# Performance work log

Hardware: AMD Instinct MI355X
Metric: run time of the kernel (lower is better)

Reference implementation:

```python
import jax, jax.numpy as jnp
import numpy as np

N_HEADS = 8
WINDOW = 64
NEG = -1e9


def _layer_norm(x, g, b, eps=1e-5):
    mu = jnp.mean(x, axis=-1, keepdims=True)
    var = jnp.mean((x - mu) ** 2, axis=-1, keepdims=True)
    return g * (x - mu) / jnp.sqrt(var + eps) + b


def _sinusoidal_pe(S, D):
    pos = jnp.arange(S, dtype=jnp.float32)[:, None]
    div = jnp.exp(jnp.arange(0, D, 2, dtype=jnp.float32) * (-jnp.log(jnp.float32(10000.0)) / D))
    pe = jnp.zeros((S, D), jnp.float32)
    pe = pe.at[:, 0::2].set(jnp.sin(pos * div))
    pe = pe.at[:, 1::2].set(jnp.cos(pos * div))
    return pe


def setup_inputs():
    key = jax.random.key(0)
    ks = jax.random.split(key, 8)
    L, S, D, DFF = 4, 2048, 1024, 2048
    p = lambda k, shape: jax.random.normal(k, shape, jnp.float32) * 0.02
    return {
        "T": 1800,
        "enc_inputs": jax.random.normal(ks[0], (1, S, D), jnp.float32),
        "global_idx": jax.random.randint(ks[1], (32,), 0, 27000),
        "Wq": p(ks[2], (L, D, D)),
        "Wk": p(ks[3], (L, D, D)),
        "Wv": p(ks[4], (L, D, D)),
        "Wo": p(ks[5], (L, D, D)),
        "ln1_g": jnp.ones((L, D), jnp.float32),
        "ln1_b": jnp.zeros((L, D), jnp.float32),
        "W1": p(ks[6], (L, D, DFF)),
        "W2": p(ks[7], (L, DFF, D)),
        "ln2_g": jnp.ones((L, D), jnp.float32),
        "ln2_b": jnp.zeros((L, D), jnp.float32),
    }


def reference(T, enc_inputs, global_idx, Wq, Wk, Wv, Wo, ln1_g, ln1_b, W1, W2, ln2_g, ln2_b):
    B, S, D = enc_inputs.shape
    L = Wq.shape[0]
    H, DK = N_HEADS, D // N_HEADS

    # enc_outputs = enc_inputs + PE(enc_inputs) = 2*enc_inputs + pe (faithful to source)
    pe = _sinusoidal_pe(S, D)
    x = enc_inputs + (enc_inputs + pe[None])

    # mask vector: 1 = local token, -1 = global token, 0 = pad
    idx = jnp.arange(S)
    mvec = jnp.where(idx < T, 1.0, 0.0)
    g = global_idx // 15
    valid = (g >= 0) & (g < S)
    is_global = jnp.any((idx[None, :] == g[:, None]) & valid[:, None], axis=0)
    mvec = jnp.where(is_global, jnp.float32(-1.0), mvec)

    half = WINDOW // 2
    local = jnp.abs(idx[:, None] - idx[None, :]) <= half
    nonpad = mvec != 0.0
    glob = mvec == -1.0
    allowed = nonpad[:, None] & nonpad[None, :] & (local | glob[:, None] | glob[None, :])
    scale = 1.0 / jnp.sqrt(jnp.float32(DK))

    for l in range(L):
        # local-global multi-head self-attention
        q = (x @ Wq[l]).reshape(B, S, H, DK).transpose(0, 2, 1, 3)
        k = (x @ Wk[l]).reshape(B, S, H, DK).transpose(0, 2, 1, 3)
        v = (x @ Wv[l]).reshape(B, S, H, DK).transpose(0, 2, 1, 3)
        scores = jnp.einsum("bhqd,bhkd->bhqk", q, k) * scale
        scores = jnp.where(allowed[None, None], scores, jnp.float32(NEG))
        attn = jax.nn.softmax(scores, axis=-1)
        ctx = jnp.einsum("bhqk,bhkd->bhqd", attn, v).transpose(0, 2, 1, 3).reshape(B, S, D)
        x = _layer_norm(ctx @ Wo[l] + x, ln1_g[l], ln1_b[l])
        # position-wise FFN with residual + LayerNorm
        h = jax.nn.relu(x @ W1[l]) @ W2[l]
        x = _layer_norm(h + x, ln2_g[l], ln2_b[l])

    return x[0]  # squeeze(0): (S, D)
```

## Files before the change

kernel.cpp:

```cpp
#include <hip/hip_runtime.h>
#include <cstdint>
#include <cstddef>

#define S_LEN  2048
#define D_MODEL 1024
#define D_FF   2048
#define NLAYER 4

typedef float  f32x4  __attribute__((ext_vector_type(4)));
typedef __bf16 bf16x8 __attribute__((ext_vector_type(8)));

#define ATT_SCALE 0.08838834764831845f

__device__ __forceinline__ void async_copy16(const void* g, void* s) {
    __builtin_amdgcn_global_load_lds((const __attribute__((address_space(1))) void*)g,
                                     (__attribute__((address_space(3))) void*)s, 16, 0, 0);
}

template<int NW>
__device__ __forceinline__ float blockRedSum(float v, float* red) {
    #pragma unroll
    for (int off = 32; off > 0; off >>= 1) v += __shfl_down(v, off);
    const int t = threadIdx.x;
    if ((t & 63) == 0) red[t >> 6] = v;
    __syncthreads();
    float r = red[0];
    #pragma unroll
    for (int i = 1; i < NW; i++) r += red[i];
    __syncthreads();
    return r;
}

__global__ __launch_bounds__(256)
void init_mask_kernel(const float* __restrict__ enc, float* __restrict__ x,
                      __bf16* __restrict__ xb, const int* __restrict__ gidx,
                      int* __restrict__ isg, int* __restrict__ gcols, int* __restrict__ ngc) {
    const int t = threadIdx.x;
    if (blockIdx.x < S_LEN) {
        const int s = blockIdx.x;
        #pragma unroll
        for (int i = 0; i < 4; i++) {
            const int d = t + i * 256;
            const float freq = expf(-(float)(d & ~1) * (9.210340371976184f / 1024.0f));
            const float ang = (float)s * freq;
            const float pe = (d & 1) ? cosf(ang) : sinf(ang);
            const float v = 2.0f * enc[(size_t)s * D_MODEL + d] + pe;
            x[(size_t)s * D_MODEL + d] = v;
            xb[(size_t)s * D_MODEL + d] = (__bf16)v;
        }
    } else {
        __shared__ int gsh[32];
        __shared__ int cnt;
        if (t < 32) {
            const int g = gidx[t] / 15;
            gsh[t] = (g >= 0 && g < S_LEN) ? g : -1;
        }
        if (t == 0) cnt = 0;
        __syncthreads();
        #pragma unroll
        for (int i = 0; i < 8; i++) {
            const int s = t + i * 256;
            int f = 0;
            #pragma unroll
            for (int j = 0; j < 32; j++) f |= (gsh[j] == s) ? 1 : 0;
            isg[s] = f;
            if (f) { const int p = atomicAdd(&cnt, 1); gcols[p] = s; }
        }
        __syncthreads();
        if (t == 0) *ngc = cnt;
    }
}

__global__ __launch_bounds__(256)
void transpose_all_kernel(const float* __restrict__ Wq, const float* __restrict__ Wk,
                          const float* __restrict__ Wv, const float* __restrict__ Wo,
                          const float* __restrict__ W1, const float* __restrict__ W2,
                          __bf16* __restrict__ out, float* __restrict__ vmean) {
    int bid = blockIdx.x;
    if (bid < 4) vmean[bid * 256 + threadIdx.x] = 0.0f;
    const float* in; __bf16* o; int K, N, r;
    if (bid < 4096) {
        const int m = bid >> 10; r = bid & 1023; K = 1024; N = 1024;
        in = (m == 0) ? Wq : (m == 1) ? Wk : (m == 2) ? Wv : Wo;
        o  = out + (size_t)m * 1024 * 1024;
    } else {
        bid -= 4096;
        const int m = bid >> 11; r = bid & 2047;
        if (m == 0) { in = W1; K = 1024; N = 2048; o = out + (size_t)4 * 1024 * 1024; }
        else        { in = W2; K = 2048; N = 1024; o = out + (size_t)6 * 1024 * 1024; }
    }
    const int ntx = N >> 5;
    const int n0 = (r % ntx) * 32, k0 = (r / ntx) * 32;
    __shared__ float tile[32][33];
    const int tx = threadIdx.x & 31, ty = threadIdx.x >> 5;
    #pragma unroll
    for (int i = ty; i < 32; i += 8)
        tile[i][tx] = in[(size_t)(k0 + i) * N + n0 + tx];
    __syncthreads();
    #pragma unroll
    for (int i = ty; i < 32; i += 8)
        o[(size_t)(n0 + i) * K + k0 + tx] = (__bf16)tile[tx][i];
}

template<int BM, int BN, int EPI, bool VACC>
__global__ __launch_bounds__(256)
void gemm_bt(const __bf16* __restrict__ A, const __bf16* __restrict__ Bt,
             void* __restrict__ Cv, float* __restrict__ vmean, int M, int N, int K) {
    constexpr int WM = BM / 2, WN = BN / 2;
    constexpr int MI = WM / 16, NI = WN / 16;
    __shared__ __bf16 As[BM * 64];
    __shared__ __bf16 Bs[BN * 64];
    const int t = threadIdx.x;
    const int w = t >> 6, l = t & 63;
    const int l15 = l & 15, q4 = l >> 4;
    const int wr = w >> 1, wc = w & 1;
    const int m0 = blockIdx.y * BM, n0 = blockIdx.x * BN;

    const int srow = t >> 3;
    const int kc8  = (t & 7) * 8;
    const __bf16* ag = A  + (size_t)(m0 + srow) * K + kc8;
    const __bf16* bg = Bt + (size_t)(n0 + srow) * K + kc8;
    __bf16* asw = As + w * 512;
    __bf16* bsw = Bs + w * 512;

    const int aoff = (wr * WM + l15) * 64 + q4 * 8;
    const int boff = (wc * WN + l15) * 64 + q4 * 8;

    f32x4 acc[MI][NI];
    #pragma unroll
    for (int i = 0; i < MI; i++)
        #pragma unroll
        for (int j = 0; j < NI; j++) acc[i][j] = (f32x4){0.f, 0.f, 0.f, 0.f};

    for (int k0 = 0; k0 < K; k0 += 64) {
        async_copy16(ag + k0, asw);
        async_copy16(ag + (size_t)32 * K + k0, asw + 2048);
        if constexpr (BM == 128) {
            async_copy16(ag + (size_t)64 * K + k0, asw + 4096);
            async_copy16(ag + (size_t)96 * K + k0, asw + 6144);
        }
        async_copy16(bg + k0, bsw);
        async_copy16(bg + (size_t)32 * K + k0, bsw + 2048);
        if constexpr (BN == 128) {
            async_copy16(bg + (size_t)64 * K + k0, bsw + 4096);
            async_copy16(bg + (size_t)96 * K + k0, bsw + 6144);
        }
        __syncthreads();
        #pragma unroll
        for (int s = 0; s < 64; s += 32) {
            bf16x8 af[MI], bfr[NI];
            #pragma unroll
            for (int i = 0; i < MI; i++) af[i]  = *(const bf16x8*)(As + aoff + i * 1024 + s);
            #pragma unroll
            for (int j = 0; j < NI; j++) bfr[j] = *(const bf16x8*)(Bs + boff + j * 1024 + s);
            #pragma unroll
            for (int i = 0; i < MI; i++)
                #pragma unroll
                for (int j = 0; j < NI; j++)
                    acc[i][j] = __builtin_amdgcn_mfma_f32_16x16x32_bf16(af[i], bfr[j], acc[i][j], 0, 0, 0);
        }
        __syncthreads();
    }

    const int r0 = m0 + wr * WM + q4 * 4;
    const int c0 = n0 + wc * WN + l15;
    if constexpr (EPI == 0) {
        float* C = (float*)Cv;
        #pragma unroll
        for (int i = 0; i < MI; i++)
            #pragma unroll
            for (int j = 0; j < NI; j++)
                #pragma unroll
                for (int r = 0; r < 4; r++)
                    C[(size_t)(r0 + i * 16 + r) * N + c0 + j * 16] = acc[i][j][r];
    } else if constexpr (EPI == 1) {
        __bf16* C = (__bf16*)Cv;
        #pragma unroll
// ... 12 lines not shown
                #pragma unroll
                for (int r = 0; r < 4; r++)
                    C[(size_t)(r0 + i * 16 + r) * N + c0 + j * 16] = (__bf16)acc[i][j][r];
    }
    if constexpr (VACC) {
        #pragma unroll
        for (int j = 0; j < NI; j++) {
            const int col = c0 + j * 16;
            if (col >= 2048) {
                float s = 0.f;
                #pragma unroll
                for (int i = 0; i < MI; i++)
                    #pragma unroll
                    for (int r = 0; r < 4; r++) s += acc[i][j][r];
                s += __shfl_xor(s, 16);
                s += __shfl_xor(s, 32);
                if (q4 == 0) atomicAdd(&vmean[col - 2048], s);
            }
        }
    }
}

__global__ __launch_bounds__(256)
void attn_local(const __bf16* __restrict__ qkvb, const int* __restrict__ Tp,
                const int* __restrict__ isg, const int* __restrict__ gcols,
                const int* __restrict__ ngcp, const float* __restrict__ vmean,
                __bf16* __restrict__ ctx) {
    const int qt0 = blockIdx.x * 32, h = blockIdx.y, hd = h * 128;
    const int t = threadIdx.x;
    __shared__ __bf16 Qs[32 * 136];
    __shared__ __bf16 Ks[128 * 136];
    __shared__ __bf16 Vs[128 * 136];
    __shared__ __bf16 Ps[32 * 136];
    __shared__ float  Ss[32 * 129];
    __shared__ int cix[128], cgf[128], rtype[32];
    __shared__ int ncs;
    const int T = *Tp, ng = *ngcp;
    const int wl = max(qt0 - 32, 0), wh = min(qt0 + 63, S_LEN - 1);
    if (t == 0) ncs = 0;
    if (t < 32) { const int qr = qt0 + t; rtype[t] = isg[qr] ? 1 : (qr < T ? 0 : 2); }
    __syncthreads();
    if (t <= wh - wl) {
        const int c = wl + t, gf = isg[c];
        if (c < T || gf) { const int p = atomicAdd(&ncs, 1); cix[p] = c; cgf[p] = gf; }
    }
    if (t < ng) {
        const int c = gcols[t];
        if (c < wl || c > wh) { const int p = atomicAdd(&ncs, 1); cix[p] = c; cgf[p] = 1; }
    }
    {
        const int r = t >> 3, d0 = (t & 7) * 16;
        const bf16x8* src = (const bf16x8*)(qkvb + (size_t)(qt0 + r) * 3072 + hd + d0);
        *(bf16x8*)&Qs[r * 136 + d0]     = src[0];
        *(bf16x8*)&Qs[r * 136 + d0 + 8] = src[1];
    }
    __syncthreads();
    const int nc = ncs;
    if (nc + t < 128) { cix[nc + t] = -1; cgf[nc + t] = 0; }
    {
        const int j = t >> 1, d0 = (t & 1) * 64;
        const int ci = (j < nc) ? cix[j] : -1;
        if (ci >= 0) {
            const bf16x8* kp = (const bf16x8*)(qkvb + (size_t)ci * 3072 + 1024 + hd + d0);
            const bf16x8* vp = (const bf16x8*)(qkvb + (size_t)ci * 3072 + 2048 + hd + d0);
            #pragma unroll
            for (int i = 0; i < 8; i++) {
                *(bf16x8*)&Ks[j * 136 + d0 + i * 8] = kp[i];
                *(bf16x8*)&Vs[j * 136 + d0 + i * 8] = vp[i];
            }
        } else {
            #pragma unroll
            for (int i = 0; i < 8; i++) {
                *(bf16x8*)&Ks[j * 136 + d0 + i * 8] = (bf16x8)(__bf16)0.f;
                *(bf16x8*)&Vs[j * 136 + d0 + i * 8] = (bf16x8)(__bf16)0.f;
            }
        }
    }
    __syncthreads();

    const int l = t & 63, w = t >> 6;
    const int l15 = l & 15, q4 = l >> 4;
    const int nb = w * 32;
    {
        f32x4 sacc[2][2];
        #pragma unroll
        for (int i = 0; i < 2; i++)
            #pragma unroll
            for (int j = 0; j < 2; j++) sacc[i][j] = (f32x4){0.f, 0.f, 0.f, 0.f};
        #pragma unroll
        for (int kk = 0; kk < 4; kk++) {
            const int k0 = kk * 32;
            bf16x8 af[2], bk[2];
            af[0] = *(const bf16x8*)&Qs[l15 * 136 + k0 + q4 * 8];
            af[1] = *(const bf16x8*)&Qs[(16 + l15) * 136 + k0 + q4 * 8];
            bk[0] = *(const bf16x8*)&Ks[(nb + l15) * 136 + k0 + q4 * 8];
            bk[1] = *(const bf16x8*)&Ks[(nb + 16 + l15) * 136 + k0 + q4 * 8];
            #pragma unroll
            for (int m2 = 0; m2 < 2; m2++)
                #pragma unroll
                for (int n2 = 0; n2 < 2; n2++)
                    sacc[m2][n2] = __builtin_amdgcn_mfma_f32_16x16x32_bf16(af[m2], bk[n2], sacc[m2][n2], 0, 0, 0);
        }
        #pragma unroll
        for (int m2 = 0; m2 < 2; m2++)
            #pragma unroll
            for (int n2 = 0; n2 < 2; n2++)
                #pragma unroll
                for (int r = 0; r < 4; r++) {
                    const int row = m2 * 16 + q4 * 4 + r;
                    const int col = nb + n2 * 16 + l15;
                    const int c = cix[col];
                    const int dd = qt0 + row - c;
                    const bool ok = (c >= 0) && (((unsigned)(dd + 32) <= 64u) || cgf[col]);
                    Ss[row * 129 + col] = ok ? sacc[m2][n2][r] * ATT_SCALE : -1e30f;
                }
    }
    __syncthreads();
    {
        const int r = t >> 3, i = t & 7;
        float mx = -1e30f;
        for (int c = i; c < 128; c += 8) mx = fmaxf(mx, Ss[r * 129 + c]);
        #pragma unroll
        for (int off = 4; off > 0; off >>= 1) mx = fmaxf(mx, __shfl_down(mx, off, 8));
        mx = __shfl(mx, 0, 8);
        float sm = 0.f;
        for (int c = i; c < 128; c += 8) {
            const float s = Ss[r * 129 + c];
            const float p = (s > -1e29f) ? __expf(s - mx) : 0.f;
            Ss[r * 129 + c] = p;
            sm += p;
        }
        #pragma unroll
        for (int off = 4; off > 0; off >>= 1) sm += __shfl_down(sm, off, 8);
        sm = __shfl(sm, 0, 8);
        const float rl = 1.0f / fmaxf(sm, 1e-30f);
        for (int c = i; c < 128; c += 8) Ps[r * 136 + c] = (__bf16)(Ss[r * 129 + c] * rl);
    }
    __syncthreads();
    {
        f32x4 oacc[2][2];
        #pragma unroll
        for (int i = 0; i < 2; i++)
            #pragma unroll
            for (int j = 0; j < 2; j++) oacc[i][j] = (f32x4){0.f, 0.f, 0.f, 0.f};
        #pragma unroll
        for (int kk = 0; kk < 4; kk++) {
            const int k0 = kk * 32;
            bf16x8 ap[2], bv[2];
            ap[0] = *(const bf16x8*)&Ps[l15 * 136 + k0 + q4 * 8];
            ap[1] = *(const bf16x8*)&Ps[(16 + l15) * 136 + k0 + q4 * 8];
            #pragma unroll
            for (int n2 = 0; n2 < 2; n2++) {
                const int dimn = nb + n2 * 16 + l15;
                #pragma unroll
                for (int jj = 0; jj < 8; jj++)
                    bv[n2][jj] = Vs[(k0 + q4 * 8 + jj) * 136 + dimn];
            }
            #pragma unroll
            for (int m2 = 0; m2 < 2; m2++)
                #pragma unroll
                for (int n2 = 0; n2 < 2; n2++)
                    oacc[m2][n2] = __builtin_amdgcn_mfma_f32_16x16x32_bf16(ap[m2], bv[n2], oacc[m2][n2], 0, 0, 0);
        }
        #pragma unroll
        for (int m2 = 0; m2 < 2; m2++)
            #pragma unroll
            for (int n2 = 0; n2 < 2; n2++)
                #pragma unroll
                for (int r = 0; r < 4; r++) {
                    const int row = m2 * 16 + q4 * 4 + r;
                    const int dim = nb + n2 * 16 + l15;
                    const int rt = rtype[row];
                    const size_t o = (size_t)(qt0 + row) * D_MODEL + hd + dim;
                    if (rt == 0)      ctx[o] = (__bf16)oacc[m2][n2][r];
                    else if (rt == 2) ctx[o] = (__bf16)(vmean[hd + dim] * (1.0f / 2048.0f));
                }
    }
}

__global__ __launch_bounds__(256)
void attn_gpart(const __bf16* __restrict__ qkvb, const int* __restrict__ Tp,
                const int* __restrict__ isg, const int* __restrict__ gcols,
                const int* __restrict__ ngcp, float* __restrict__ Og,
                float* __restrict__ mg, float* __restrict__ lg) {
    const int cb = blockIdx.x, h = blockIdx.y, hd = h * 128, c0 = cb * 128;
    const int t = threadIdx.x;
    const int ng = *ngcp, T = *Tp;
    if (ng == 0) return;
    __shared__ __bf16 Qs[32 * 136];
    __shared__ __bf16 Ks[128 * 136];
    __shared__ __bf16 Vs[128 * 136];
    __shared__ __bf16 Ps[32 * 136];
    __shared__ float  Ss[32 * 129];
    __shared__ int vf[128];
    {
        const int r = t >> 3, d0 = (t & 7) * 16;
        if (r < ng) {
            const bf16x8* src = (const bf16x8*)(qkvb + (size_t)gcols[r] * 3072 + hd + d0);
            *(bf16x8*)&Qs[r * 136 + d0]     = src[0];
            *(bf16x8*)&Qs[r * 136 + d0 + 8] = src[1];
        } else {
            *(bf16x8*)&Qs[r * 136 + d0]     = (bf16x8)(__bf16)0.f;
            *(bf16x8*)&Qs[r * 136 + d0 + 8] = (bf16x8)(__bf16)0.f;
        }
    }
    if (t < 128) { const int c = c0 + t; vf[t] = (c < T || isg[c]) ? 1 : 0; }
    {
        const int j = t >> 1, d0 = (t & 1) * 64;
        const int ci = c0 + j;
        const bf16x8* kp = (const bf16x8*)(qkvb + (size_t)ci * 3072 + 1024 + hd + d0);
        const bf16x8* vp = (const bf16x8*)(qkvb + (size_t)ci * 3072 + 2048 + hd + d0);
        #pragma unroll
        for (int i = 0; i < 8; i++) {
            *(bf16x8*)&Ks[j * 136 + d0 + i * 8] = kp[i];
            *(bf16x8*)&Vs[j * 136 + d0 + i * 8] = vp[i];
        }
    }
    __syncthreads();

    const int l = t & 63, w = t >> 6;
    const int l15 = l & 15, q4 = l >> 4;
    const int nb = w * 32;
    {
        f32x4 sacc[2][2];
        #pragma unroll
        for (int i = 0; i < 2; i++)
            #pragma unroll
            for (int j = 0; j < 2; j++) sacc[i][j] = (f32x4){0.f, 0.f, 0.f, 0.f};
        #pragma unroll
        for (int kk = 0; kk < 4; kk++) {
            const int k0 = kk * 32;
            bf16x8 af[2], bk[2];
            af[0] = *(const bf16x8*)&Qs[l15 * 136 + k0 + q4 * 8];
            af[1] = *(const bf16x8*)&Qs[(16 + l15) * 136 + k0 + q4 * 8];
            bk[0] = *(const bf16x8*)&Ks[(nb + l15) * 136 + k0 + q4 * 8];
            bk[1] = *(const bf16x8*)&Ks[(nb + 16 + l15) * 136 + k0 + q4 * 8];
            #pragma unroll
            for (int m2 = 0; m2 < 2; m2++)
                #pragma unroll
                for (int n2 = 0; n2 < 2; n2++)
                    sacc[m2][n2] = __builtin_amdgcn_mfma_f32_16x16x32_bf16(af[m2], bk[n2], sacc[m2][n2], 0, 0, 0);
        }
        #pragma unroll
        for (int m2 = 0; m2 < 2; m2++)
            #pragma unroll
            for (int n2 = 0; n2 < 2; n2++)
                #pragma unroll
                for (int r = 0; r < 4; r++) {
                    const int row = m2 * 16 + q4 * 4 + r;
                    const int col = nb + n2 * 16 + l15;
                    Ss[row * 129 + col] = vf[col] ? sacc[m2][n2][r] * ATT_SCALE : -1e30f;
                }
    }
    __syncthreads();
    {
        const int r = t >> 3, i = t & 7;
        float mx = -1e30f;
        for (int c = i; c < 128; c += 8) mx = fmaxf(mx, Ss[r * 129 + c]);
        #pragma unroll
        for (int off = 4; off > 0; off >>= 1) mx = fmaxf(mx, __shfl_down(mx, off, 8));
        mx = __shfl(mx, 0, 8);
        float sm = 0.f;
        for (int c = i; c < 128; c += 8) {
            const float s = Ss[r * 129 + c];
            const float p = (s > -1e29f) ? __expf(s - mx) : 0.f;
            Ps[r * 136 + c] = (__bf16)p;
            sm += p;
        }
        #pragma unroll
        for (int off = 4; off > 0; off >>= 1) sm += __shfl_down(sm, off, 8);
        if (i == 0) { mg[(h * 16 + cb) * 32 + r] = mx; lg[(h * 16 + cb) * 32 + r] = sm; }
    }
    __syncthreads();
    {
        f32x4 oacc[2][2];
        #pragma unroll
        for (int i = 0; i < 2; i++)
            #pragma unroll
            for (int j = 0; j < 2; j++) oacc[i][j] = (f32x4){0.f, 0.f, 0.f, 0.f};
        #pragma unroll
        for (int kk = 0; kk < 4; kk++) {
            const int k0 = kk * 32;
            bf16x8 ap[2], bv[2];
            ap[0] = *(const bf16x8*)&Ps[l15 * 136 + k0 + q4 * 8];
            ap[1] = *(const bf16x8*)&Ps[(16 + l15) * 136 + k0 + q4 * 8];
            #pragma unroll
            for (int n2 = 0; n2 < 2; n2++) {
                const int dimn = nb + n2 * 16 + l15;
                #pragma unroll
                for (int jj = 0; jj < 8; jj++)
                    bv[n2][jj] = Vs[(k0 + q4 * 8 + jj) * 136 + dimn];
            }
            #pragma unroll
            for (int m2 = 0; m2 < 2; m2++)
                #pragma unroll
                for (int n2 = 0; n2 < 2; n2++)
                    oacc[m2][n2] = __builtin_amdgcn_mfma_f32_16x16x32_bf16(ap[m2], bv[n2], oacc[m2][n2], 0, 0, 0);
        }
        #pragma unroll
        for (int m2 = 0; m2 < 2; m2++)
            #pragma unroll
            for (int n2 = 0; n2 < 2; n2++)
                #pragma unroll
                for (int r = 0; r < 4; r++) {
                    const int row = m2 * 16 + q4 * 4 + r;
                    const int dim = nb + n2 * 16 + l15;
                    Og[((size_t)(h * 16 + cb) * 32 + row) * 128 + dim] = oacc[m2][n2][r];
                }
    }
}

__global__ __launch_bounds__(256)
void attn_gcomb(const int* __restrict__ gcols, const int* __restrict__ ngcp,
                const float* __restrict__ Og, const float* __restrict__ mg,
                const float* __restrict__ lg, __bf16* __restrict__ ctx) {
    const int h = blockIdx.x, hd = h * 128, t = threadIdx.x;
    const int ng = *ngcp;
    const int r = t >> 3, i = t & 7;
    if (r >= ng) return;
    float M = -1e30f;
    #pragma unroll
    for (int cb = 0; cb < 16; cb++) M = fmaxf(M, mg[(h * 16 + cb) * 32 + r]);
    float e[16], L = 0.f;
    #pragma unroll
    for (int cb = 0; cb < 16; cb++) {
        e[cb] = __expf(mg[(h * 16 + cb) * 32 + r] - M);
        L += e[cb] * lg[(h * 16 + cb) * 32 + r];
    }
    const float rL = 1.0f / fmaxf(L, 1e-30f);
    const int grow = gcols[r];
    for (int d = i; d < 128; d += 8) {
        float o = 0.f;
        #pragma unroll
        for (int cb = 0; cb < 16; cb++)
            o += e[cb] * Og[((size_t)(h * 16 + cb) * 32 + r) * 128 + d];
        ctx[(size_t)grow * D_MODEL + hd + d] = (__bf16)(o * rL);
    }
}

__global__ __launch_bounds__(256)
void ln_kernel(const float* __restrict__ y, const float* __restrict__ r,
               const float* __restrict__ g, const float* __restrict__ b,
               float* __restrict__ xo, __bf16* __restrict__ xb) {
    const int row = blockIdx.x, t = threadIdx.x;
    const float* yr = y + (size_t)row * D_MODEL;
    const float* rr = r + (size_t)row * D_MODEL;
    __shared__ float red[4];
    float v[4]; float s = 0.f;
    #pragma unroll
    for (int i = 0; i < 4; i++) { const int d = t + i * 256; v[i] = yr[d] + rr[d]; s += v[i]; }
    s = blockRedSum<4>(s, red);
    const float mu = s * (1.0f / 1024.0f);
    float vs = 0.f;
    #pragma unroll
    for (int i = 0; i < 4; i++) { const float dd = v[i] - mu; vs += dd * dd; }
    vs = blockRedSum<4>(vs, red);
    const float rstd = rsqrtf(vs * (1.0f / 1024.0f) + 1e-5f);
    #pragma unroll
    for (int i = 0; i < 4; i++) {
        const int d = t + i * 256;
        const float o = g[d] * (v[i] - mu) * rstd + b[d];
        xo[(size_t)row * D_MODEL + d] = o;
        xb[(size_t)row * D_MODEL + d] = (__bf16)o;
    }
}

extern "C" void kernel_launch(void* const* d_in, const int* in_sizes, int n_in,
// ... 6 lines not shown
    const float* Wk   = (const float*)d_in[4];
    const float* Wv   = (const float*)d_in[5];
    const float* Wo   = (const float*)d_in[6];
    const float* ln1g = (const float*)d_in[7];
    const float* ln1b = (const float*)d_in[8];
    const float* W1   = (const float*)d_in[9];
    const float* W2   = (const float*)d_in[10];
    const float* ln2g = (const float*)d_in[11];
    const float* ln2b = (const float*)d_in[12];

    char* p = (char*)d_ws;
    size_t off = 0;
    auto alloc = [&](size_t bytes) -> void* {
        void* q = p + off;
        off += (bytes + 255) & ~(size_t)255;
        return q;
    };
    float*  x     = (float*) alloc((size_t)S_LEN * D_MODEL * 4);
    __bf16* xb    = (__bf16*)alloc((size_t)S_LEN * D_MODEL * 2);
    __bf16* qkvb  = (__bf16*)alloc((size_t)S_LEN * 3072 * 2);
    __bf16* ctx   = (__bf16*)alloc((size_t)S_LEN * D_MODEL * 2);
    float*  g1    = (float*) alloc((size_t)S_LEN * D_MODEL * 4);
    __bf16* h1    = (__bf16*)alloc((size_t)S_LEN * D_FF * 2);
    __bf16* wT    = (__bf16*)alloc((size_t)8 * 1024 * 1024 * 2);
    float*  vmean = (float*) alloc(1024 * 4);
    int*    isg   = (int*)   alloc(S_LEN * 4);
    int*    gcols = (int*)   alloc(S_LEN * 4);
    int*    ngc   = (int*)   alloc(256);
    float*  Og    = (float*) alloc((size_t)8 * 16 * 32 * 128 * 4);
    float*  mgb   = (float*) alloc(8 * 16 * 32 * 4);
    float*  lgb   = (float*) alloc(8 * 16 * 32 * 4);

    init_mask_kernel<<<S_LEN + 1, 256, 0, stream>>>(enc, x, xb, gidx, isg, gcols, ngc);

    for (int l = 0; l < NLAYER; l++) {
        const size_t lw = (size_t)l * 1024 * 1024;
        const size_t lf = (size_t)l * 1024 * 2048;
        transpose_all_kernel<<<8192, 256, 0, stream>>>(Wq + lw, Wk + lw, Wv + lw, Wo + lw,
                                                       W1 + lf, W2 + lf, wT, vmean);
        gemm_bt<64, 128, 2, true><<<dim3(24, 32), 256, 0, stream>>>(xb, wT, (void*)qkvb, vmean, S_LEN, 3072, 1024);

        attn_local<<<dim3(64, 8), 256, 0, stream>>>(qkvb, Tp, isg, gcols, ngc, vmean, ctx);
        attn_gpart<<<dim3(16, 8), 256, 0, stream>>>(qkvb, Tp, isg, gcols, ngc, Og, mgb, lgb);
        attn_gcomb<<<8, 256, 0, stream>>>(gcols, ngc, Og, mgb, lgb, ctx);

        gemm_bt<64, 64, 0, false><<<dim3(16, 32), 256, 0, stream>>>(ctx, wT + (size_t)3 * 1024 * 1024, (void*)g1, nullptr, S_LEN, 1024, 1024);
        ln_kernel<<<S_LEN, 256, 0, stream>>>(g1, x, ln1g + l * 1024, ln1b + l * 1024, x, xb);

        gemm_bt<64, 64, 1, false><<<dim3(32, 32), 256, 0, stream>>>(xb, wT + (size_t)4 * 1024 * 1024, (void*)h1, nullptr, S_LEN, 2048, 1024);
        gemm_bt<64, 64, 0, false><<<dim3(16, 32), 256, 0, stream>>>(h1, wT + (size_t)6 * 1024 * 1024, (void*)g1, nullptr, S_LEN, 1024, 2048);
        float* xout = (l == NLAYER - 1) ? (float*)d_out : x;
        ln_kernel<<<S_LEN, 256, 0, stream>>>(g1, x, ln2g + l * 1024, ln2b + l * 1024, xout, xb);
    }
}
```

Baseline: 768.6 us.

## Batch weight transposes, fuse attention kernels, and deepen GEMM K-tile

Transposes all four layers' weights in one upfront launch into a larger arena instead of once per layer. The local and global-partial attention kernels are merged into a single launch, and vmean zeroing moves into the init and LayerNorm kernels. The GEMM K-tile grows from 64 to 128 through a new template parameter. These cut launch count and per-iteration sync overhead, but the larger LDS tiles may lower occupancy and the weight arena now takes four times the memory.

```diff
diff --git a/kernel.cpp b/kernel.cpp
--- a/kernel.cpp
+++ b/kernel.cpp
@@ -34,7 +34,8 @@
 __global__ __launch_bounds__(256)
 void init_mask_kernel(const float* __restrict__ enc, float* __restrict__ x,
                       __bf16* __restrict__ xb, const int* __restrict__ gidx,
-                      int* __restrict__ isg, int* __restrict__ gcols, int* __restrict__ ngc) {
+                      int* __restrict__ isg, int* __restrict__ gcols, int* __restrict__ ngc,
+                      float* __restrict__ vmean) {
     const int t = threadIdx.x;
     if (blockIdx.x < S_LEN) {
         const int s = blockIdx.x;
@@ -49,6 +50,8 @@
             xb[(size_t)s * D_MODEL + d] = (__bf16)v;
         }
     } else {
+        #pragma unroll
+        for (int i = 0; i < 4; i++) vmean[t + i * 256] = 0.0f;
         __shared__ int gsh[32];
         __shared__ int cnt;
         if (t < 32) {
@@ -75,19 +78,22 @@
 void transpose_all_kernel(const float* __restrict__ Wq, const float* __restrict__ Wk,
                           const float* __restrict__ Wv, const float* __restrict__ Wo,
                           const float* __restrict__ W1, const float* __restrict__ W2,
-                          __bf16* __restrict__ out, float* __restrict__ vmean) {
-    int bid = blockIdx.x;
-    if (bid < 4) vmean[bid * 256 + threadIdx.x] = 0.0f;
+                          __bf16* __restrict__ out) {
+    const int layer = blockIdx.x >> 13;
+    int bid = blockIdx.x & 8191;
+    const size_t lw = (size_t)layer * 1024 * 1024;
+    const size_t lf = (size_t)layer * 1024 * 2048;
+    __bf16* arena = out + (size_t)layer * 8 * 1024 * 1024;
     const float* in; __bf16* o; int K, N, r;
     if (bid < 4096) {
         const int m = bid >> 10; r = bid & 1023; K = 1024; N = 1024;
-        in = (m == 0) ? Wq : (m == 1) ? Wk : (m == 2) ? Wv : Wo;
-        o  = out + (size_t)m * 1024 * 1024;
+        in = ((m == 0) ? Wq : (m == 1) ? Wk : (m == 2) ? Wv : Wo) + lw;
+        o  = arena + (size_t)m * 1024 * 1024;
     } else {
         bid -= 4096;
         const int m = bid >> 11; r = bid & 2047;
-        if (m == 0) { in = W1; K = 1024; N = 2048; o = out + (size_t)4 * 1024 * 1024; }
-        else        { in = W2; K = 2048; N = 1024; o = out + (size_t)6 * 1024 * 1024; }
+        if (m == 0) { in = W1 + lf; K = 1024; N = 2048; o = arena + (size_t)4 * 1024 * 1024; }
+        else        { in = W2 + lf; K = 2048; N = 1024; o = arena + (size_t)6 * 1024 * 1024; }
     }
     const int ntx = N >> 5;
     const int n0 = (r % ntx) * 32, k0 = (r / ntx) * 32;
@@ -102,29 +108,32 @@
         o[(size_t)(n0 + i) * K + k0 + tx] = (__bf16)tile[tx][i];
 }
 
-template<int BM, int BN, int EPI, bool VACC>
+template<int BM, int BN, int BK, int EPI, bool VACC>
 __global__ __launch_bounds__(256)
 void gemm_bt(const __bf16* __restrict__ A, const __bf16* __restrict__ Bt,
              void* __restrict__ Cv, float* __restrict__ vmean, int M, int N, int K) {
     constexpr int WM = BM / 2, WN = BN / 2;
     constexpr int MI = WM / 16, NI = WN / 16;
-    __shared__ __bf16 As[BM * 64];
-    __shared__ __bf16 Bs[BN * 64];
+    constexpr int TPR = BK / 8;
+    constexpr int RPR = 2048 / BK;
+    constexpr int RA = BM / RPR, RB = BN / RPR;
+    __shared__ __bf16 As[BM * BK];
+    __shared__ __bf16 Bs[BN * BK];
     const int t = threadIdx.x;
     const int w = t >> 6, l = t & 63;
     const int l15 = l & 15, q4 = l >> 4;
     const int wr = w >> 1, wc = w & 1;
     const int m0 = blockIdx.y * BM, n0 = blockIdx.x * BN;
 
-    const int srow = t >> 3;
-    const int kc8  = (t & 7) * 8;
+    const int srow = t / TPR;
+    const int kc8  = (t % TPR) * 8;
     const __bf16* ag = A  + (size_t)(m0 + srow) * K + kc8;
     const __bf16* bg = Bt + (size_t)(n0 + srow) * K + kc8;
     __bf16* asw = As + w * 512;
     __bf16* bsw = Bs + w * 512;
 
-    const int aoff = (wr * WM + l15) * 64 + q4 * 8;
-    const int boff = (wc * WN + l15) * 64 + q4 * 8;
+    const int aoff = (wr * WM + l15) * BK + q4 * 8;
+    const int boff = (wc * WN + l15) * BK + q4 * 8;
 
     f32x4 acc[MI][NI];
     #pragma unroll
@@ -132,27 +141,21 @@
         #pragma unroll
         for (int j = 0; j < NI; j++) acc[i][j] = (f32x4){0.f, 0.f, 0.f, 0.f};
 
-    for (int k0 = 0; k0 < K; k0 += 64) {
-        async_copy16(ag + k0, asw);
-        async_copy16(ag + (size_t)32 * K + k0, asw + 2048);
-        if constexpr (BM == 128) {
-            async_copy16(ag + (size_t)64 * K + k0, asw + 4096);
-            async_copy16(ag + (size_t)96 * K + k0, asw + 6144);
-        }
-        async_copy16(bg + k0, bsw);
-        async_copy16(bg + (size_t)32 * K + k0, bsw + 2048);
-        if constexpr (BN == 128) {
-            async_copy16(bg + (size_t)64 * K + k0, bsw + 4096);
-            async_copy16(bg + (size_t)96 * K + k0, bsw + 6144);
-        }
-        __syncthreads();
-        #pragma unroll
-        for (int s = 0; s < 64; s += 32) {
+    for (int k0 = 0; k0 < K; k0 += BK) {
+        #pragma unroll
+        for (int rr = 0; rr < RA; rr++)
+            async_copy16(ag + (size_t)rr * RPR * K + k0, asw + rr * 2048);
+        #pragma unroll
+        for (int rr = 0; rr < RB; rr++)
+            async_copy16(bg + (size_t)rr * RPR * K + k0, bsw + rr * 2048);
+        __syncthreads();
+        #pragma unroll
+        for (int s = 0; s < BK; s += 32) {
             bf16x8 af[MI], bfr[NI];
             #pragma unroll
-            for (int i = 0; i < MI; i++) af[i]  = *(const bf16x8*)(As + aoff + i * 1024 + s);
-            #pragma unroll
-            for (int j = 0; j < NI; j++) bfr[j] = *(const bf16x8*)(Bs + boff + j * 1024 + s);
+            for (int i = 0; i < MI; i++) af[i]  = *(const bf16x8*)(As + aoff + i * 16 * BK + s);
+            #pragma unroll
+            for (int j = 0; j < NI; j++) bfr[j] = *(const bf16x8*)(Bs + boff + j * 16 * BK + s);
             #pragma unroll
             for (int i = 0; i < MI; i++)
                 #pragma unroll
@@ -211,12 +214,14 @@
 }
 
 __global__ __launch_bounds__(256)
-void attn_local(const __bf16* __restrict__ qkvb, const int* __restrict__ Tp,
-                const int* __restrict__ isg, const int* __restrict__ gcols,
-                const int* __restrict__ ngcp, const float* __restrict__ vmean,
-                __bf16* __restrict__ ctx) {
-    const int qt0 = blockIdx.x * 32, h = blockIdx.y, hd = h * 128;
+void attn_kernel(const __bf16* __restrict__ qkvb, const int* __restrict__ Tp,
+                 const int* __restrict__ isg, const int* __restrict__ gcols,
+                 const int* __restrict__ ngcp, const float* __restrict__ vmean,
+                 __bf16* __restrict__ ctx, float* __restrict__ Og,
+                 float* __restrict__ mg, float* __restrict__ lg) {
+    const int h = blockIdx.y, hd = h * 128;
     const int t = threadIdx.x;
+    const int T = *Tp, ng = *ngcp;
     __shared__ __bf16 Qs[32 * 136];
     __shared__ __bf16 Ks[128 * 136];
     __shared__ __bf16 Vs[128 * 136];
@@ -224,32 +229,166 @@
     __shared__ float  Ss[32 * 129];
     __shared__ int cix[128], cgf[128], rtype[32];
     __shared__ int ncs;
-    const int T = *Tp, ng = *ngcp;
-    const int wl = max(qt0 - 32, 0), wh = min(qt0 + 63, S_LEN - 1);
-    if (t == 0) ncs = 0;
-    if (t < 32) { const int qr = qt0 + t; rtype[t] = isg[qr] ? 1 : (qr < T ? 0 : 2); }
-    __syncthreads();
-    if (t <= wh - wl) {
-        const int c = wl + t, gf = isg[c];
-        if (c < T || gf) { const int p = atomicAdd(&ncs, 1); cix[p] = c; cgf[p] = gf; }
-    }
-    if (t < ng) {
-        const int c = gcols[t];
-        if (c < wl || c > wh) { const int p = atomicAdd(&ncs, 1); cix[p] = c; cgf[p] = 1; }
-    }
-    {
-        const int r = t >> 3, d0 = (t & 7) * 16;
-        const bf16x8* src = (const bf16x8*)(qkvb + (size_t)(qt0 + r) * 3072 + hd + d0);
-        *(bf16x8*)&Qs[r * 136 + d0]     = src[0];
-        *(bf16x8*)&Qs[r * 136 + d0 + 8] = src[1];
-    }
-    __syncthreads();
-    const int nc = ncs;
-    if (nc + t < 128) { cix[nc + t] = -1; cgf[nc + t] = 0; }
-    {
-        const int j = t >> 1, d0 = (t & 1) * 64;
-        const int ci = (j < nc) ? cix[j] : -1;
-        if (ci >= 0) {
+    const int l = t & 63, w = t >> 6;
+    const int l15 = l & 15, q4 = l >> 4;
+    const int nb = w * 32;
+
+    if (blockIdx.x < 64) {
+        const int qt0 = blockIdx.x * 32;
+        const int wl = max(qt0 - 32, 0), wh = min(qt0 + 63, S_LEN - 1);
+        if (t == 0) ncs = 0;
+        if (t < 32) { const int qr = qt0 + t; rtype[t] = isg[qr] ? 1 : (qr < T ? 0 : 2); }
+        __syncthreads();
+        if (t <= wh - wl) {
+            const int c = wl + t, gf = isg[c];
+            if (c < T || gf) { const int p = atomicAdd(&ncs, 1); cix[p] = c; cgf[p] = gf; }
+        }
+        if (t < ng) {
+            const int c = gcols[t];
+            if (c < wl || c > wh) { const int p = atomicAdd(&ncs, 1); cix[p] = c; cgf[p] = 1; }
+        }
+        {
+            const int r = t >> 3, d0 = (t & 7) * 16;
+            const bf16x8* src = (const bf16x8*)(qkvb + (size_t)(qt0 + r) * 3072 + hd + d0);
+            *(bf16x8*)&Qs[r * 136 + d0]     = src[0];
+            *(bf16x8*)&Qs[r * 136 + d0 + 8] = src[1];
+        }
+        __syncthreads();
+        const int nc = ncs;
+        if (nc + t < 128) { cix[nc + t] = -1; cgf[nc + t] = 0; }
+        {
+            const int j = t >> 1, d0 = (t & 1) * 64;
+            const int ci = (j < nc) ? cix[j] : -1;
+            if (ci >= 0) {
+                const bf16x8* kp = (const bf16x8*)(qkvb + (size_t)ci * 3072 + 1024 + hd + d0);
+                const bf16x8* vp = (const bf16x8*)(qkvb + (size_t)ci * 3072 + 2048 + hd + d0);
+                #pragma unroll
+                for (int i = 0; i < 8; i++) {
+                    *(bf16x8*)&Ks[j * 136 + d0 + i * 8] = kp[i];
+                    *(bf16x8*)&Vs[j * 136 + d0 + i * 8] = vp[i];
+                }
+            } else {
+                #pragma unroll
+                for (int i = 0; i < 8; i++) {
+                    *(bf16x8*)&Ks[j * 136 + d0 + i * 8] = (bf16x8)(__bf16)0.f;
+                    *(bf16x8*)&Vs[j * 136 + d0 + i * 8] = (bf16x8)(__bf16)0.f;
+                }
+            }
+        }
+        __syncthreads();
+        {
+            f32x4 sacc[2][2];
+            #pragma unroll
+            for (int i = 0; i < 2; i++)
+                #pragma unroll
+                for (int j = 0; j < 2; j++) sacc[i][j] = (f32x4){0.f, 0.f, 0.f, 0.f};
+            #pragma unroll
+            for (int kk = 0; kk < 4; kk++) {
+                const int k0 = kk * 32;
+                bf16x8 af[2], bk[2];
+                af[0] = *(const bf16x8*)&Qs[l15 * 136 + k0 + q4 * 8];
+                af[1] = *(const bf16x8*)&Qs[(16 + l15) * 136 + k0 + q4 * 8];
+                bk[0] = *(const bf16x8*)&Ks[(nb + l15) * 136 + k0 + q4 * 8];
+                bk[1] = *(const bf16x8*)&Ks[(nb + 16 + l15) * 136 + k0 + q4 * 8];
+                #pragma unroll
+                for (int m2 = 0; m2 < 2; m2++)
+                    #pragma unroll
+                    for (int n2 = 0; n2 < 2; n2++)
+                        sacc[m2][n2] = __builtin_amdgcn_mfma_f32_16x16x32_bf16(af[m2], bk[n2], sacc[m2][n2], 0, 0, 0);
+            }
+            #pragma unroll
+            for (int m2 = 0; m2 < 2; m2++)
+                #pragma unroll
+                for (int n2 = 0; n2 < 2; n2++)
+                    #pragma unroll
+                    for (int r = 0; r < 4; r++) {
+                        const int row = m2 * 16 + q4 * 4 + r;
+                        const int col = nb + n2 * 16 + l15;
+                        const int c = cix[col];
+                        const int dd = qt0 + row - c;
+                        const bool ok = (c >= 0) && (((unsigned)(dd + 32) <= 64u) || cgf[col]);
+                        Ss[row * 129 + col] = ok ? sacc[m2][n2][r] * ATT_SCALE : -1e30f;
+                    }
+        }
+        __syncthreads();
+        {
+            const int r = t >> 3, i = t & 7;
+            float mx = -1e30f;
+            for (int c = i; c < 128; c += 8) mx = fmaxf(mx, Ss[r * 129 + c]);
+            #pragma unroll
+            for (int off = 4; off > 0; off >>= 1) mx = fmaxf(mx, __shfl_down(mx, off, 8));
+            mx = __shfl(mx, 0, 8);
+            float sm = 0.f;
+            for (int c = i; c < 128; c += 8) {
+                const float s = Ss[r * 129 + c];
+                const float p = (s > -1e29f) ? __expf(s - mx) : 0.f;
+                Ss[r * 129 + c] = p;
+                sm += p;
+            }
+            #pragma unroll
+            for (int off = 4; off > 0; off >>= 1) sm += __shfl_down(sm, off, 8);
+            sm = __shfl(sm, 0, 8);
+            const float rl = 1.0f / fmaxf(sm, 1e-30f);
+            for (int c = i; c < 128; c += 8) Ps[r * 136 + c] = (__bf16)(Ss[r * 129 + c] * rl);
+        }
+        __syncthreads();
+        {
+            f32x4 oacc[2][2];
+            #pragma unroll
+            for (int i = 0; i < 2; i++)
+                #pragma unroll
+                for (int j = 0; j < 2; j++) oacc[i][j] = (f32x4){0.f, 0.f, 0.f, 0.f};
+            #pragma unroll
+            for (int kk = 0; kk < 4; kk++) {
+                const int k0 = kk * 32;
+                bf16x8 ap[2], bv[2];
+                ap[0] = *(const bf16x8*)&Ps[l15 * 136 + k0 + q4 * 8];
+                ap[1] = *(const bf16x8*)&Ps[(16 + l15) * 136 + k0 + q4 * 8];
+                #pragma unroll
+                for (int n2 = 0; n2 < 2; n2++) {
+                    const int dimn = nb + n2 * 16 + l15;
+                    #pragma unroll
+                    for (int jj = 0; jj < 8; jj++)
+                        bv[n2][jj] = Vs[(k0 + q4 * 8 + jj) * 136 + dimn];
+                }
+                #pragma unroll
+                for (int m2 = 0; m2 < 2; m2++)
+                    #pragma unroll
+                    for (int n2 = 0; n2 < 2; n2++)
+                        oacc[m2][n2] = __builtin_amdgcn_mfma_f32_16x16x32_bf16(ap[m2], bv[n2], oacc[m2][n2], 0, 0, 0);
+            }
+            #pragma unroll
+            for (int m2 = 0; m2 < 2; m2++)
+                #pragma unroll
+                for (int n2 = 0; n2 < 2; n2++)
+                    #pragma unroll
+                    for (int r = 0; r < 4; r++) {
+                        const int row = m2 * 16 + q4 * 4 + r;
+                        const int dim = nb + n2 * 16 + l15;
+                        const int rt = rtype[row];
+                        const size_t o = (size_t)(qt0 + row) * D_MODEL + hd + dim;
+                        if (rt == 0)      ctx[o] = (__bf16)oacc[m2][n2][r];
+                        else if (rt == 2) ctx[o] = (__bf16)(vmean[hd + dim] * (1.0f / 2048.0f));
+                    }
+        }
+    } else {
+        if (ng == 0) return;
+        const int cb = blockIdx.x - 64, c0 = cb * 128;
+        {
+            const int r = t >> 3, d0 = (t & 7) * 16;
+            if (r < ng) {
+                const bf16x8* src = (const bf16x8*)(qkvb + (size_t)gcols[r] * 3072 + hd + d0);
+                *(bf16x8*)&Qs[r * 136 + d0]     = src[0];
+                *(bf16x8*)&Qs[r * 136 + d0 + 8] = src[1];
+            } else {
+                *(bf16x8*)&Qs[r * 136 + d0]     = (bf16x8)(__bf16)0.f;
+                *(bf16x8*)&Qs[r * 136 + d0 + 8] = (bf16x8)(__bf16)0.f;
+            }
+        }
+        if (t < 128) { const int c = c0 + t; cix[t] = (c < T || isg[c]) ? 1 : 0; }
+        {
+            const int j = t >> 1, d0 = (t & 1) * 64;
+            const int ci = c0 + j;
             const bf16x8* kp = (const bf16x8*)(qkvb + (size_t)ci * 3072 + 1024 + hd + d0);
             const bf16x8* vp = (const bf16x8*)(qkvb + (size_t)ci * 3072 + 2048 + hd + d0);
             #pragma unroll
@@ -257,245 +396,95 @@
                 *(bf16x8*)&Ks[j * 136 + d0 + i * 8] = kp[i];
                 *(bf16x8*)&Vs[j * 136 + d0 + i * 8] = vp[i];
             }
-        } else {
-            #pragma unroll
-            for (int i = 0; i < 8; i++) {
-                *(bf16x8*)&Ks[j * 136 + d0 + i * 8] = (bf16x8)(__bf16)0.f;
-                *(bf16x8*)&Vs[j * 136 + d0 + i * 8] = (bf16x8)(__bf16)0.f;
-            }
-        }
-    }
-    __syncthreads();
-
-    const int l = t & 63, w = t >> 6;
-    const int l15 = l & 15, q4 = l >> 4;
-    const int nb = w * 32;
-    {
-        f32x4 sacc[2][2];
-        #pragma unroll
-        for (int i = 0; i < 2; i++)
-            #pragma unroll
-            for (int j = 0; j < 2; j++) sacc[i][j] = (f32x4){0.f, 0.f, 0.f, 0.f};
-        #pragma unroll
-        for (int kk = 0; kk < 4; kk++) {
-            const int k0 = kk * 32;
-            bf16x8 af[2], bk[2];
-            af[0] = *(const bf16x8*)&Qs[l15 * 136 + k0 + q4 * 8];
-            af[1] = *(const bf16x8*)&Qs[(16 + l15) * 136 + k0 + q4 * 8];
-            bk[0] = *(const bf16x8*)&Ks[(nb + l15) * 136 + k0 + q4 * 8];
-            bk[1] = *(const bf16x8*)&Ks[(nb + 16 + l15) * 136 + k0 + q4 * 8];
+        }
+        __syncthreads();
+        {
+            f32x4 sacc[2][2];
+            #pragma unroll
+            for (int i = 0; i < 2; i++)
+                #pragma unroll
+                for (int j = 0; j < 2; j++) sacc[i][j] = (f32x4){0.f, 0.f, 0.f, 0.f};
+            #pragma unroll
+            for (int kk = 0; kk < 4; kk++) {
+                const int k0 = kk * 32;
+                bf16x8 af[2], bk[2];
+                af[0] = *(const bf16x8*)&Qs[l15 * 136 + k0 + q4 * 8];
+                af[1] = *(const bf16x8*)&Qs[(16 + l15) * 136 + k0 + q4 * 8];
+                bk[0] = *(const bf16x8*)&Ks[(nb + l15) * 136 + k0 + q4 * 8];
+                bk[1] = *(const bf16x8*)&Ks[(nb + 16 + l15) * 136 + k0 + q4 * 8];
+                #pragma unroll
+                for (int m2 = 0; m2 < 2; m2++)
+                    #pragma unroll
+                    for (int n2 = 0; n2 < 2; n2++)
+                        sacc[m2][n2] = __builtin_amdgcn_mfma_f32_16x16x32_bf16(af[m2], bk[n2], sacc[m2][n2], 0, 0, 0);
+            }
             #pragma unroll
             for (int m2 = 0; m2 < 2; m2++)
                 #pragma unroll
                 for (int n2 = 0; n2 < 2; n2++)
-                    sacc[m2][n2] = __builtin_amdgcn_mfma_f32_16x16x32_bf16(af[m2], bk[n2], sacc[m2][n2], 0, 0, 0);
-        }
-        #pragma unroll
-        for (int m2 = 0; m2 < 2; m2++)
-            #pragma unroll
-            for (int n2 = 0; n2 < 2; n2++)
-                #pragma unroll
-                for (int r = 0; r < 4; r++) {
-                    const int row = m2 * 16 + q4 * 4 + r;
-                    const int col = nb + n2 * 16 + l15;
-                    const int c = cix[col];
-                    const int dd = qt0 + row - c;
-                    const bool ok = (c >= 0) && (((unsigned)(dd + 32) <= 64u) || cgf[col]);
-                    Ss[row * 129 + col] = ok ? sacc[m2][n2][r] * ATT_SCALE : -1e30f;
+                    #pragma unroll
+                    for (int r = 0; r < 4; r++) {
+                        const int row = m2 * 16 + q4 * 4 + r;
+                        const int col = nb + n2 * 16 + l15;
+                        Ss[row * 129 + col] = cix[col] ? sacc[m2][n2][r] * ATT_SCALE : -1e30f;
+                    }
+        }
+        __syncthreads();
+        {
+            const int r = t >> 3, i = t & 7;
+            float mx = -1e30f;
+            for (int c = i; c < 128; c += 8) mx = fmaxf(mx, Ss[r * 129 + c]);
+            #pragma unroll
+            for (int off = 4; off > 0; off >>= 1) mx = fmaxf(mx, __shfl_down(mx, off, 8));
+            mx = __shfl(mx, 0, 8);
+            float sm = 0.f;
+            for (int c = i; c < 128; c += 8) {
+                const float s = Ss[r * 129 + c];
+                const float p = (s > -1e29f) ? __expf(s - mx) : 0.f;
+                Ps[r * 136 + c] = (__bf16)p;
+                sm += p;
+            }
+            #pragma unroll
+            for (int off = 4; off > 0; off >>= 1) sm += __shfl_down(sm, off, 8);
+            if (i == 0) { mg[(h * 16 + cb) * 32 + r] = mx; lg[(h * 16 + cb) * 32 + r] = sm; }
+        }
+        __syncthreads();
+        {
+            f32x4 oacc[2][2];
+            #pragma unroll
+            for (int i = 0; i < 2; i++)
+                #pragma unroll
+                for (int j = 0; j < 2; j++) oacc[i][j] = (f32x4){0.f, 0.f, 0.f, 0.f};
+            #pragma unroll
+            for (int kk = 0; kk < 4; kk++) {
+                const int k0 = kk * 32;
+                bf16x8 ap[2], bv[2];
+                ap[0] = *(const bf16x8*)&Ps[l15 * 136 + k0 + q4 * 8];
+                ap[1] = *(const bf16x8*)&Ps[(16 + l15) * 136 + k0 + q4 * 8];
+                #pragma unroll
+                for (int n2 = 0; n2 < 2; n2++) {
+                    const int dimn = nb + n2 * 16 + l15;
+                    #pragma unroll
+                    for (int jj = 0; jj < 8; jj++)
+                        bv[n2][jj] = Vs[(k0 + q4 * 8 + jj) * 136 + dimn];
                 }
-    }
-    __syncthreads();
-    {
-        const int r = t >> 3, i = t & 7;
-        float mx = -1e30f;
-        for (int c = i; c < 128; c += 8) mx = fmaxf(mx, Ss[r * 129 + c]);
-        #pragma unroll
-        for (int off = 4; off > 0; off >>= 1) mx = fmaxf(mx, __shfl_down(mx, off, 8));
-        mx = __shfl(mx, 0, 8);
-        float sm = 0.f;
-        for (int c = i; c < 128; c += 8) {
-            const float s = Ss[r * 129 + c];
-            const float p = (s > -1e29f) ? __expf(s - mx) : 0.f;
-            Ss[r * 129 + c] = p;
-            sm += p;
-        }
-        #pragma unroll
-        for (int off = 4; off > 0; off >>= 1) sm += __shfl_down(sm, off, 8);
-        sm = __shfl(sm, 0, 8);
-        const float rl = 1.0f / fmaxf(sm, 1e-30f);
-        for (int c = i; c < 128; c += 8) Ps[r * 136 + c] = (__bf16)(Ss[r * 129 + c] * rl);
-    }
-    __syncthreads();
-    {
-        f32x4 oacc[2][2];
-        #pragma unroll
-        for (int i = 0; i < 2; i++)
-            #pragma unroll
-            for (int j = 0; j < 2; j++) oacc[i][j] = (f32x4){0.f, 0.f, 0.f, 0.f};
-        #pragma unroll
-        for (int kk = 0; kk < 4; kk++) {
-            const int k0 = kk * 32;
-            bf16x8 ap[2], bv[2];
-            ap[0] = *(const bf16x8*)&Ps[l15 * 136 + k0 + q4 * 8];
-            ap[1] = *(const bf16x8*)&Ps[(16 + l15) * 136 + k0 + q4 * 8];
-            #pragma unroll
-            for (int n2 = 0; n2 < 2; n2++) {
-                const int dimn = nb + n2 * 16 + l15;
-                #pragma unroll
-                for (int jj = 0; jj < 8; jj++)
-                    bv[n2][jj] = Vs[(k0 + q4 * 8 + jj) * 136 + dimn];
+                #pragma unroll
+                for (int m2 = 0; m2 < 2; m2++)
+                    #pragma unroll
+                    for (int n2 = 0; n2 < 2; n2++)
+                        oacc[m2][n2] = __builtin_amdgcn_mfma_f32_16x16x32_bf16(ap[m2], bv[n2], oacc[m2][n2], 0, 0, 0);
             }
             #pragma unroll
             for (int m2 = 0; m2 < 2; m2++)
                 #pragma unroll
                 for (int n2 = 0; n2 < 2; n2++)
-                    oacc[m2][n2] = __builtin_amdgcn_mfma_f32_16x16x32_bf16(ap[m2], bv[n2], oacc[m2][n2], 0, 0, 0);
-        }
-        #pragma unroll
-        for (int m2 = 0; m2 < 2; m2++)
-            #pragma unroll
-            for (int n2 = 0; n2 < 2; n2++)
-                #pragma unroll
-                for (int r = 0; r < 4; r++) {
-                    const int row = m2 * 16 + q4 * 4 + r;
-                    const int dim = nb + n2 * 16 + l15;
-                    const int rt = rtype[row];
-                    const size_t o = (size_t)(qt0 + row) * D_MODEL + hd + dim;
-                    if (rt == 0)      ctx[o] = (__bf16)oacc[m2][n2][r];
-                    else if (rt == 2) ctx[o] = (__bf16)(vmean[hd + dim] * (1.0f / 2048.0f));
-                }
-    }
-}
-
-__global__ __launch_bounds__(256)
-void attn_gpart(const __bf16* __restrict__ qkvb, const int* __restrict__ Tp,
-                const int* __restrict__ isg, const int* __restrict__ gcols,
-                const int* __restrict__ ngcp, float* __restrict__ Og,
-                float* __restrict__ mg, float* __restrict__ lg) {
-    const int cb = blockIdx.x, h = blockIdx.y, hd = h * 128, c0 = cb * 128;
-    const int t = threadIdx.x;
-    const int ng = *ngcp, T = *Tp;
-    if (ng == 0) return;
-    __shared__ __bf16 Qs[32 * 136];
-    __shared__ __bf16 Ks[128 * 136];
-    __shared__ __bf16 Vs[128 * 136];
-    __shared__ __bf16 Ps[32 * 136];
-    __shared__ float  Ss[32 * 129];
-    __shared__ int vf[128];
-    {
-        const int r = t >> 3, d0 = (t & 7) * 16;
-        if (r < ng) {
-            const bf16x8* src = (const bf16x8*)(qkvb + (size_t)gcols[r] * 3072 + hd + d0);
-            *(bf16x8*)&Qs[r * 136 + d0]     = src[0];
-            *(bf16x8*)&Qs[r * 136 + d0 + 8] = src[1];
-        } else {
-            *(bf16x8*)&Qs[r * 136 + d0]     = (bf16x8)(__bf16)0.f;
-            *(bf16x8*)&Qs[r * 136 + d0 + 8] = (bf16x8)(__bf16)0.f;
-        }
-    }
-    if (t < 128) { const int c = c0 + t; vf[t] = (c < T || isg[c]) ? 1 : 0; }
-    {
-        const int j = t >> 1, d0 = (t & 1) * 64;
-        const int ci = c0 + j;
-        const bf16x8* kp = (const bf16x8*)(qkvb + (size_t)ci * 3072 + 1024 + hd + d0);
-        const bf16x8* vp = (const bf16x8*)(qkvb + (size_t)ci * 3072 + 2048 + hd + d0);
-        #pragma unroll
-        for (int i = 0; i < 8; i++) {
-            *(bf16x8*)&Ks[j * 136 + d0 + i * 8] = kp[i];
-            *(bf16x8*)&Vs[j * 136 + d0 + i * 8] = vp[i];
-        }
-    }
-    __syncthreads();
-
-    const int l = t & 63, w = t >> 6;
-    const int l15 = l & 15, q4 = l >> 4;
-    const int nb = w * 32;
-    {
-        f32x4 sacc[2][2];
-        #pragma unroll
-        for (int i = 0; i < 2; i++)
-            #pragma unroll
-            for (int j = 0; j < 2; j++) sacc[i][j] = (f32x4){0.f, 0.f, 0.f, 0.f};
-        #pragma unroll
-        for (int kk = 0; kk < 4; kk++) {
-            const int k0 = kk * 32;
-            bf16x8 af[2], bk[2];
-            af[0] = *(const bf16x8*)&Qs[l15 * 136 + k0 + q4 * 8];
-            af[1] = *(const bf16x8*)&Qs[(16 + l15) * 136 + k0 + q4 * 8];
-            bk[0] = *(const bf16x8*)&Ks[(nb + l15) * 136 + k0 + q4 * 8];
-            bk[1] = *(const bf16x8*)&Ks[(nb + 16 + l15) * 136 + k0 + q4 * 8];
-            #pragma unroll
-            for (int m2 = 0; m2 < 2; m2++)
-                #pragma unroll
-                for (int n2 = 0; n2 < 2; n2++)
-                    sacc[m2][n2] = __builtin_amdgcn_mfma_f32_16x16x32_bf16(af[m2], bk[n2], sacc[m2][n2], 0, 0, 0);
-        }
-        #pragma unroll
-        for (int m2 = 0; m2 < 2; m2++)
-            #pragma unroll
-            for (int n2 = 0; n2 < 2; n2++)
-                #pragma unroll
-                for (int r = 0; r < 4; r++) {
-                    const int row = m2 * 16 + q4 * 4 + r;
-                    const int col = nb + n2 * 16 + l15;
-                    Ss[row * 129 + col] = vf[col] ? sacc[m2][n2][r] * ATT_SCALE : -1e30f;
-                }
-    }
-    __syncthreads();
-    {
-        const int r = t >> 3, i = t & 7;
-        float mx = -1e30f;
-        for (int c = i; c < 128; c += 8) mx = fmaxf(mx, Ss[r * 129 + c]);
-        #pragma unroll
-        for (int off = 4; off > 0; off >>= 1) mx = fmaxf(mx, __shfl_down(mx, off, 8));
-        mx = __shfl(mx, 0, 8);
-        float sm = 0.f;
-        for (int c = i; c < 128; c += 8) {
-            const float s = Ss[r * 129 + c];
-            const float p = (s > -1e29f) ? __expf(s - mx) : 0.f;
-            Ps[r * 136 + c] = (__bf16)p;
-            sm += p;
-        }
-        #pragma unroll
-        for (int off = 4; off > 0; off >>= 1) sm += __shfl_down(sm, off, 8);
-        if (i == 0) { mg[(h * 16 + cb) * 32 + r] = mx; lg[(h * 16 + cb) * 32 + r] = sm; }
-    }
-    __syncthreads();
-    {
-        f32x4 oacc[2][2];
-        #pragma unroll
-        for (int i = 0; i < 2; i++)
-            #pragma unroll
-            for (int j = 0; j < 2; j++) oacc[i][j] = (f32x4){0.f, 0.f, 0.f, 0.f};
-        #pragma unroll
-        for (int kk = 0; kk < 4; kk++) {
-            const int k0 = kk * 32;
-            bf16x8 ap[2], bv[2];
-            ap[0] = *(const bf16x8*)&Ps[l15 * 136 + k0 + q4 * 8];
-            ap[1] = *(const bf16x8*)&Ps[(16 + l15) * 136 + k0 + q4 * 8];
-            #pragma unroll
-            for (int n2 = 0; n2 < 2; n2++) {
-                const int dimn = nb + n2 * 16 + l15;
-                #pragma unroll
-                for (int jj = 0; jj < 8; jj++)
-                    bv[n2][jj] = Vs[(k0 + q4 * 8 + jj) * 136 + dimn];
-            }
-            #pragma unroll
-            for (int m2 = 0; m2 < 2; m2++)
-                #pragma unroll
-                for (int n2 = 0; n2 < 2; n2++)
-                    oacc[m2][n2] = __builtin_amdgcn_mfma_f32_16x16x32_bf16(ap[m2], bv[n2], oacc[m2][n2], 0, 0, 0);
-        }
-        #pragma unroll
-        for (int m2 = 0; m2 < 2; m2++)
-            #pragma unroll
-            for (int n2 = 0; n2 < 2; n2++)
-                #pragma unroll
-                for (int r = 0; r < 4; r++) {
-                    const int row = m2 * 16 + q4 * 4 + r;
-                    const int dim = nb + n2 * 16 + l15;
-                    Og[((size_t)(h * 16 + cb) * 32 + row) * 128 + dim] = oacc[m2][n2][r];
-                }
+                    #pragma unroll
+                    for (int r = 0; r < 4; r++) {
+                        const int row = m2 * 16 + q4 * 4 + r;
+                        const int dim = nb + n2 * 16 + l15;
+                        Og[((size_t)(h * 16 + cb) * 32 + row) * 128 + dim] = oacc[m2][n2][r];
+                    }
+        }
     }
 }
 
@@ -530,8 +519,12 @@
 __global__ __launch_bounds__(256)
 void ln_kernel(const float* __restrict__ y, const float* __restrict__ r,
                const float* __restrict__ g, const float* __restrict__ b,
-               float* __restrict__ xo, __bf16* __restrict__ xb) {
+               float* __restrict__ xo, __bf16* __restrict__ xb, float* __restrict__ vz) {
     const int row = blockIdx.x, t = threadIdx.x;
+    if (vz != nullptr && row == 0) {
+        #pragma unroll
+        for (int i = 0; i < 4; i++) vz[t + i * 256] = 0.0f;
+    }
     const float* yr = y + (size_t)row * D_MODEL;
     const float* rr = r + (size_t)row * D_MODEL;
     __shared__ float red[4];
@@ -584,7 +577,7 @@
     __bf16* ctx   = (__bf16*)alloc((size_t)S_LEN * D_MODEL * 2);
     float*  g1    = (float*) alloc((size_t)S_LEN * D_MODEL * 4);
     __bf16* h1    = (__bf16*)alloc((size_t)S_LEN * D_FF * 2);
-    __bf16* wT    = (__bf16*)alloc((size_t)8 * 1024 * 1024 * 2);
+    __bf16* wT    = (__bf16*)alloc((size_t)4 * 8 * 1024 * 1024 * 2);
     float*  vmean = (float*) alloc(1024 * 4);
     int*    isg   = (int*)   alloc(S_LEN * 4);
     int*    gcols = (int*)   alloc(S_LEN * 4);
@@ -593,25 +586,22 @@
     float*  mgb   = (float*) alloc(8 * 16 * 32 * 4);
     float*  lgb   = (float*) alloc(8 * 16 * 32 * 4);
 
-    init_mask_kernel<<<S_LEN + 1, 256, 0, stream>>>(enc, x, xb, gidx, isg, gcols, ngc);
+    init_mask_kernel<<<S_LEN + 1, 256, 0, stream>>>(enc, x, xb, gidx, isg, gcols, ngc, vmean);
+    transpose_all_kernel<<<32768, 256, 0, stream>>>(Wq, Wk, Wv, Wo, W1, W2, wT);
 
     for (int l = 0; l < NLAYER; l++) {
-        const size_t lw = (size_t)l * 1024 * 1024;
-        const size_t lf = (size_t)l * 1024 * 2048;
-        transpose_all_kernel<<<8192, 256, 0, stream>>>(Wq + lw, Wk + lw, Wv + lw, Wo + lw,
-                                                       W1 + lf, W2 + lf, wT, vmean);
-        gemm_bt<64, 128, 2, true><<<dim3(24, 32), 256, 0, stream>>>(xb, wT, (void*)qkvb, vmean, S_LEN, 3072, 1024);
-
-        attn_local<<<dim3(64, 8), 256, 0, stream>>>(qkvb, Tp, isg, gcols, ngc, vmean, ctx);
-        attn_gpart<<<dim3(16, 8), 256, 0, stream>>>(qkvb, Tp, isg, gcols, ngc, Og, mgb, lgb);
+        __bf16* wL = wT + (size_t)l * 8 * 1024 * 1024;
+        gemm_bt<64, 128, 128, 2, true><<<dim3(24, 32), 256, 0, stream>>>(xb, wL, (void*)qkvb, vmean, S_LEN, 3072, 1024);
+
+        attn_kernel<<<dim3(80, 8), 256, 0, stream>>>(qkvb, Tp, isg, gcols, ngc, vmean, ctx, Og, mgb, lgb);
         attn_gcomb<<<8, 256, 0, stream>>>(gcols, ngc, Og, mgb, lgb, ctx);
 
-        gemm_bt<64, 64, 0, false><<<dim3(16, 32), 256, 0, stream>>>(ctx, wT + (size_t)3 * 1024 * 1024, (void*)g1, nullptr, S_LEN, 1024, 1024);
-        ln_kernel<<<S_LEN, 256, 0, stream>>>(g1, x, ln1g + l * 1024, ln1b + l * 1024, x, xb);
-
-        gemm_bt<64, 64, 1, false><<<dim3(32, 32), 256, 0, stream>>>(xb, wT + (size_t)4 * 1024 * 1024, (void*)h1, nullptr, S_LEN, 2048, 1024);
-        gemm_bt<64, 64, 0, false><<<dim3(16, 32), 256, 0, stream>>>(h1, wT + (size_t)6 * 1024 * 1024, (void*)g1, nullptr, S_LEN, 1024, 2048);
+        gemm_bt<64, 64, 128, 0, false><<<dim3(16, 32), 256, 0, stream>>>(ctx, wL + (size_t)3 * 1024 * 1024, (void*)g1, nullptr, S_LEN, 1024, 1024);
+        ln_kernel<<<S_LEN, 256, 0, stream>>>(g1, x, ln1g + l * 1024, ln1b + l * 1024, x, xb, nullptr);
+
+        gemm_bt<64, 64, 128, 1, false><<<dim3(32, 32), 256, 0, stream>>>(xb, wL + (size_t)4 * 1024 * 1024, (void*)h1, nullptr, S_LEN, 2048, 1024);
+        gemm_bt<64, 64, 128, 0, false><<<dim3(16, 32), 256, 0, stream>>>(h1, wL + (size_t)6 * 1024 * 1024, (void*)g1, nullptr, S_LEN, 1024, 2048);
         float* xout = (l == NLAYER - 1) ? (float*)d_out : x;
-        ln_kernel<<<S_LEN, 256, 0, stream>>>(g1, x, ln2g + l * 1024, ln2b + l * 1024, xout, xb);
-    }
-}
+        ln_kernel<<<S_LEN, 256, 0, stream>>>(g1, x, ln2g + l * 1024, ln2b + l * 1024, xout, xb, vmean);
+    }
+}
```

New measurement: 909.7 us. 18.4% more time.
